# Kernel tuning notes

Hardware: AMD Instinct MI355X
Metric: run time of the kernel (lower is better)

## Reference

```python
import jax, jax.numpy as jnp
import numpy as np

E = 800_000      # number of edges
D = 256          # d_model_edge
N = 50_000       # number of atoms/nodes


def setup_inputs() -> dict:
    key = jax.random.key(0)
    k1, k2, k3, k4, k5 = jax.random.split(key, 5)
    forces = jax.random.normal(k1, (E, D), dtype=jnp.float32)
    V_st = jax.random.normal(k2, (E, 3), dtype=jnp.float32)
    # MLP([D, D, 1]): Linear(D,D) + act + Linear(D,1). Scaled init for stability.
    W1 = jax.random.normal(k3, (D, D), dtype=jnp.float32) * (1.0 / np.sqrt(D))
    b1 = jnp.zeros((D,), dtype=jnp.float32)
    W2 = jax.random.normal(k4, (D, 1), dtype=jnp.float32) * (1.0 / np.sqrt(D))
    b2 = jnp.zeros((1,), dtype=jnp.float32)
    idx_t = jax.random.randint(k5, (E,), 0, N, dtype=jnp.int64 if jax.config.jax_enable_x64 else jnp.int32)
    return {
        "forces": forces,
        "V_st": V_st,
        "W1": W1,
        "b1": b1,
        "W2": W2,
        "b2": b2,
        "idx_t": idx_t,
        "n_atoms": N,
    }


def reference(forces, V_st, W1, b1, W2, b2, idx_t, n_atoms):
    # out_mlp: Linear(D,D) -> SiLU -> Linear(D,1)
    h = jax.nn.silu(forces @ W1 + b1)          # [E, D]
    s = h @ W2 + b2                            # [E, 1] per-edge scalar
    ev = s * V_st                              # [E, 3] scaled direction vectors
    # scatter-sum over target node indices (reduction='sum')
    out = jax.ops.segment_sum(ev, idx_t, num_segments=n_atoms)  # [N, 3]
    return out
```

## Files before the change

kernel.cpp:

```cpp
#include <hip/hip_runtime.h>
#include <hip/hip_bf16.h>

typedef __attribute__((ext_vector_type(8))) short short8;
typedef __attribute__((ext_vector_type(4))) float floatx4;
typedef unsigned short u16;

#define D 256
#define BM 64
#define NT 256

__device__ __forceinline__ short f2bf(float f) {
    return __builtin_bit_cast(short, __float2bfloat16(f));
}

__global__ void prep_kernel(const float* __restrict__ W1, u16* __restrict__ W1F,
                            float* __restrict__ out, int outn) {
    const int b = blockIdx.x;
    if (b < D) {
        const int k = b, n = threadIdx.x;
        const int k0t = k >> 5, g = (k >> 3) & 3, j = k & 7;
        const int nt = n >> 4, l15 = n & 15;
        W1F[(long)((((k0t << 4) + nt) << 6) + (g << 4) + l15) * 8 + j] = (u16)f2bf(W1[k * D + n]);
    } else {
        int i = (b - D) * 256 + threadIdx.x;
        const int stride = (gridDim.x - D) * 256;
        for (; i < outn; i += stride) out[i] = 0.f;
    }
}

struct R8 { floatx4 f0, f1; };

__launch_bounds__(NT, 4)
__global__ void head_kernel(const float* __restrict__ forces,
                            const float* __restrict__ V_st,
                            const u16*   __restrict__ W1F,
                            const float* __restrict__ b1,
                            const float* __restrict__ W2,
                            const float* __restrict__ b2,
                            const int*   __restrict__ idx_t,
                            float* __restrict__ out,
                            int E) {
    __shared__ u16 Albs[32 * 512];
    __shared__ float s_red[2][BM];

    const int tid  = threadIdx.x;
    const int lane = tid & 63;
    const int w    = tid >> 6;
    const int wm   = w >> 1;
    const int wn   = w & 1;
    const int l15  = lane & 15;
    const int g    = lane >> 4;

    const long t = blockIdx.x;
    const long row0 = t * BM;

    float vx = 0.f, vy = 0.f, vz = 0.f;
    int node = -1;
    if (tid < BM) {
        long e = row0 + tid;
        if (e < E) {
            vx = V_st[e * 3 + 0]; vy = V_st[e * 3 + 1]; vz = V_st[e * 3 + 2];
            node = idx_t[e];
        }
    }

    const int arow = tid >> 2;
    const int agg  = tid & 3;
    long grow = row0 + arow;
    if (grow > (long)E - 1) grow = (long)E - 1;
    const float* abase = forces + grow * D + agg * 8;

    R8 r[8];
#pragma unroll
    for (int k0t = 0; k0t < 8; ++k0t) {
        r[k0t].f0 = *(const floatx4*)(abase + k0t * 32);
        r[k0t].f1 = *(const floatx4*)(abase + k0t * 32 + 4);
    }
    const int aslot = ((agg << 4) | (arow & 15)) * 8;
    const int art   = arow >> 4;
#pragma unroll
    for (int k0t = 0; k0t < 8; ++k0t) {
        short8 a;
#pragma unroll
        for (int j = 0; j < 4; ++j) { a[j] = f2bf(r[k0t].f0[j]); a[4 + j] = f2bf(r[k0t].f1[j]); }
        *(short8*)&Albs[(k0t * 4 + art) * 512 + aslot] = a;
    }
    __syncthreads();

    floatx4 acc[2][8];
#pragma unroll
    for (int mr = 0; mr < 2; ++mr)
#pragma unroll
        for (int nc = 0; nc < 8; ++nc)
            acc[mr][nc] = (floatx4){0.f, 0.f, 0.f, 0.f};

#pragma unroll
    for (int k0t = 0; k0t < 8; ++k0t) {
        short8 bf[8], af[2];
#pragma unroll
        for (int nc = 0; nc < 8; ++nc)
            bf[nc] = *(const short8*)(W1F + (long)((k0t * 16 + wn * 8 + nc) * 64 + lane) * 8);
#pragma unroll
        for (int mr = 0; mr < 2; ++mr)
            af[mr] = *(const short8*)&Albs[(k0t * 4 + wm * 2 + mr) * 512 + lane * 8];
#pragma unroll
        for (int mr = 0; mr < 2; ++mr)
#pragma unroll
            for (int nc = 0; nc < 8; ++nc)
                acc[mr][nc] = __builtin_amdgcn_mfma_f32_16x16x32_bf16(
                    af[mr], bf[nc], acc[mr][nc], 0, 0, 0);
    }

    float b1v[8], w2v[8];
#pragma unroll
    for (int nc = 0; nc < 8; ++nc) {
        int n = wn * 128 + nc * 16 + l15;
        b1v[nc] = b1[n];
        w2v[nc] = W2[n];
    }
    float part[2][4];
#pragma unroll
    for (int mr = 0; mr < 2; ++mr)
#pragma unroll
        for (int rr = 0; rr < 4; ++rr) {
            float sv = 0.f;
#pragma unroll
            for (int nc = 0; nc < 8; ++nc) {
                float z = acc[mr][nc][rr] + b1v[nc];
                float h = z / (1.f + __expf(-z));
                sv += h * w2v[nc];
            }
            part[mr][rr] = sv;
        }

#pragma unroll
    for (int off = 1; off < 16; off <<= 1)
#pragma unroll
        for (int mr = 0; mr < 2; ++mr)
#pragma unroll
            for (int rr = 0; rr < 4; ++rr)
                part[mr][rr] += __shfl_xor(part[mr][rr], off, 16);

    if (l15 == 0) {
#pragma unroll
        for (int mr = 0; mr < 2; ++mr)
#pragma unroll
            for (int rr = 0; rr < 4; ++rr)
                s_red[wn][wm * 32 + mr * 16 + g * 4 + rr] = part[mr][rr];
    }
    __syncthreads();

    if (node >= 0) {
        float sv = s_red[0][tid] + s_red[1][tid] + b2[0];
        atomicAdd(&out[(long)node * 3 + 0], sv * vx);
        atomicAdd(&out[(long)node * 3 + 1], sv * vy);
        atomicAdd(&out[(long)node * 3 + 2], sv * vz);
    }
}

extern "C" void kernel_launch(void* const* d_in, const int* in_sizes, int n_in,
                              void* d_out, int out_size, void* d_ws, size_t ws_size,
                              hipStream_t stream) {
    const float* forces = (const float*)d_in[0];
    const float* V_st   = (const float*)d_in[1];
    const float* W1     = (const float*)d_in[2];
    const float* b1     = (const float*)d_in[3];
    const float* W2     = (const float*)d_in[4];
    const float* b2     = (const float*)d_in[5];
    const int*   idx    = (const int*)d_in[6];
    const int E = in_sizes[6];

    u16* W1F = (u16*)d_ws;

    prep_kernel<<<D + 128, 256, 0, stream>>>(W1, W1F, (float*)d_out, out_size);
    const int grid = (E + BM - 1) / BM;
    head_kernel<<<grid, NT, 0, stream>>>(forces, V_st, W1F, b1, W2, b2, idx,
                                         (float*)d_out, E);
}
```

Measured before the change: 282.1 us.

## Shrink head tile to 32 rows with one wave per 16 rows owning all columns

Halves the block to 32 edges and 128 threads, and gives each wave all 256 output columns for its 16 rows. This removes the cross-wave reduction through shared memory and the second barrier, so each wave does its own atomic scatter. Forces are now read with nontemporal loads, and the tail clamp and bounds checks are dropped, which assumes E is a multiple of 32. The trade-off is that each wave now fetches every W1 fragment itself and holds 16 accumulators, which raises W1 reloads per edge and register pressure.

Result: slower. 388.7 us (+37.8%).

```diff
diff --git a/kernel.cpp b/kernel.cpp
--- a/kernel.cpp
+++ b/kernel.cpp
@@ -6,8 +6,8 @@
 typedef unsigned short u16;
 
 #define D 256
-#define BM 64
-#define NT 256
+#define BM 32
+#define NT 128
 
 __device__ __forceinline__ short f2bf(float f) {
     return __builtin_bit_cast(short, __float2bfloat16(f));
@@ -28,8 +28,6 @@
     }
 }
 
-struct R8 { floatx4 f0, f1; };
-
 __launch_bounds__(NT, 4)
 __global__ void head_kernel(const float* __restrict__ forces,
                             const float* __restrict__ V_st,
@@ -40,41 +38,38 @@
                             const int*   __restrict__ idx_t,
                             float* __restrict__ out,
                             int E) {
-    __shared__ u16 Albs[32 * 512];
-    __shared__ float s_red[2][BM];
+    __shared__ u16 Albs[16 * 512];
 
     const int tid  = threadIdx.x;
     const int lane = tid & 63;
-    const int w    = tid >> 6;
-    const int wm   = w >> 1;
-    const int wn   = w & 1;
+    const int wm   = tid >> 6;
     const int l15  = lane & 15;
     const int g    = lane >> 4;
 
-    const long t = blockIdx.x;
-    const long row0 = t * BM;
+    const long row0 = (long)blockIdx.x * BM;
 
-    float vx = 0.f, vy = 0.f, vz = 0.f;
-    int node = -1;
-    if (tid < BM) {
-        long e = row0 + tid;
-        if (e < E) {
-            vx = V_st[e * 3 + 0]; vy = V_st[e * 3 + 1]; vz = V_st[e * 3 + 2];
-            node = idx_t[e];
+    float vx[4], vy[4], vz[4];
+    int nd[4];
+    if (l15 == 0) {
+#pragma unroll
+        for (int rr = 0; rr < 4; ++rr) {
+            long e = row0 + wm * 16 + g * 4 + rr;
+            vx[rr] = V_st[e * 3 + 0];
+            vy[rr] = V_st[e * 3 + 1];
+            vz[rr] = V_st[e * 3 + 2];
+            nd[rr] = idx_t[e];
         }
     }
 
     const int arow = tid >> 2;
     const int agg  = tid & 3;
-    long grow = row0 + arow;
-    if (grow > (long)E - 1) grow = (long)E - 1;
-    const float* abase = forces + grow * D + agg * 8;
+    const float* abase = forces + (row0 + arow) * D + agg * 8;
 
-    R8 r[8];
+    floatx4 f0[8], f1[8];
 #pragma unroll
     for (int k0t = 0; k0t < 8; ++k0t) {
-        r[k0t].f0 = *(const floatx4*)(abase + k0t * 32);
-        r[k0t].f1 = *(const floatx4*)(abase + k0t * 32 + 4);
+        f0[k0t] = __builtin_nontemporal_load((const floatx4*)(abase + k0t * 32));
+        f1[k0t] = __builtin_nontemporal_load((const floatx4*)(abase + k0t * 32 + 4));
     }
     const int aslot = ((agg << 4) | (arow & 15)) * 8;
     const int art   = arow >> 4;
@@ -82,79 +77,54 @@
     for (int k0t = 0; k0t < 8; ++k0t) {
         short8 a;
 #pragma unroll
-        for (int j = 0; j < 4; ++j) { a[j] = f2bf(r[k0t].f0[j]); a[4 + j] = f2bf(r[k0t].f1[j]); }
-        *(short8*)&Albs[(k0t * 4 + art) * 512 + aslot] = a;
+        for (int j = 0; j < 4; ++j) { a[j] = f2bf(f0[k0t][j]); a[4 + j] = f2bf(f1[k0t][j]); }
+        *(short8*)&Albs[(k0t * 2 + art) * 512 + aslot] = a;
     }
     __syncthreads();
 
-    floatx4 acc[2][8];
+    floatx4 acc[16];
 #pragma unroll
-    for (int mr = 0; mr < 2; ++mr)
-#pragma unroll
-        for (int nc = 0; nc < 8; ++nc)
-            acc[mr][nc] = (floatx4){0.f, 0.f, 0.f, 0.f};
+    for (int nc = 0; nc < 16; ++nc)
+        acc[nc] = (floatx4){0.f, 0.f, 0.f, 0.f};
 
 #pragma unroll
     for (int k0t = 0; k0t < 8; ++k0t) {
-        short8 bf[8], af[2];
+        short8 af = *(const short8*)&Albs[(k0t * 2 + wm) * 512 + lane * 8];
 #pragma unroll
-        for (int nc = 0; nc < 8; ++nc)
-            bf[nc] = *(const short8*)(W1F + (long)((k0t * 16 + wn * 8 + nc) * 64 + lane) * 8);
-#pragma unroll
-        for (int mr = 0; mr < 2; ++mr)
-            af[mr] = *(const short8*)&Albs[(k0t * 4 + wm * 2 + mr) * 512 + lane * 8];
-#pragma unroll
-        for (int mr = 0; mr < 2; ++mr)
-#pragma unroll
-            for (int nc = 0; nc < 8; ++nc)
-                acc[mr][nc] = __builtin_amdgcn_mfma_f32_16x16x32_bf16(
-                    af[mr], bf[nc], acc[mr][nc], 0, 0, 0);
+        for (int nc = 0; nc < 16; ++nc) {
+            short8 bf = *(const short8*)(W1F + (long)((k0t * 16 + nc) * 64 + lane) * 8);
+            acc[nc] = __builtin_amdgcn_mfma_f32_16x16x32_bf16(af, bf, acc[nc], 0, 0, 0);
+        }
     }
 
-    float b1v[8], w2v[8];
+    float part[4];
 #pragma unroll
-    for (int nc = 0; nc < 8; ++nc) {
-        int n = wn * 128 + nc * 16 + l15;
-        b1v[nc] = b1[n];
-        w2v[nc] = W2[n];
+    for (int rr = 0; rr < 4; ++rr) {
+        float sv = 0.f;
+#pragma unroll
+        for (int nc = 0; nc < 16; ++nc) {
+            float z = acc[nc][rr] + b1[nc * 16 + l15];
+            float h = z / (1.f + __expf(-z));
+            sv += h * W2[nc * 16 + l15];
+        }
+        part[rr] = sv;
     }
-    float part[2][4];
-#pragma unroll
-    for (int mr = 0; mr < 2; ++mr)
-#pragma unroll
-        for (int rr = 0; rr < 4; ++rr) {
-            float sv = 0.f;
-#pragma unroll
-            for (int nc = 0; nc < 8; ++nc) {
-                float z = acc[mr][nc][rr] + b1v[nc];
-                float h = z / (1.f + __expf(-z));
-                sv += h * w2v[nc];
-            }
-            part[mr][rr] = sv;
-        }
 
 #pragma unroll
     for (int off = 1; off < 16; off <<= 1)
 #pragma unroll
-        for (int mr = 0; mr < 2; ++mr)
-#pragma unroll
-            for (int rr = 0; rr < 4; ++rr)
-                part[mr][rr] += __shfl_xor(part[mr][rr], off, 16);
+        for (int rr = 0; rr < 4; ++rr)
+            part[rr] += __shfl_xor(part[rr], off, 16);
 
     if (l15 == 0) {
+        const float b2v = b2[0];
 #pragma unroll
-        for (int mr = 0; mr < 2; ++mr)
-#pragma unroll
-            for (int rr = 0; rr < 4; ++rr)
-                s_red[wn][wm * 32 + mr * 16 + g * 4 + rr] = part[mr][rr];
-    }
-    __syncthreads();
-
-    if (node >= 0) {
-        float sv = s_red[0][tid] + s_red[1][tid] + b2[0];
-        atomicAdd(&out[(long)node * 3 + 0], sv * vx);
-        atomicAdd(&out[(long)node * 3 + 1], sv * vy);
-        atomicAdd(&out[(long)node * 3 + 2], sv * vz);
+        for (int rr = 0; rr < 4; ++rr) {
+            float sv = part[rr] + b2v;
+            atomicAdd(&out[(long)nd[rr] * 3 + 0], sv * vx[rr]);
+            atomicAdd(&out[(long)nd[rr] * 3 + 1], sv * vy[rr]);
+            atomicAdd(&out[(long)nd[rr] * 3 + 2], sv * vz[rr]);
+        }
     }
 }
 
@@ -173,7 +143,7 @@
     u16* W1F = (u16*)d_ws;
 
     prep_kernel<<<D + 128, 256, 0, stream>>>(W1, W1F, (float*)d_out, out_size);
-    const int grid = (E + BM - 1) / BM;
+    const int grid = E / BM;
     head_kernel<<<grid, NT, 0, stream>>>(forces, V_st, W1F, b1, W2, b2, idx,
                                          (float*)d_out, E);
 }
```
